# Kernel optimization log

Measured on AMD Instinct MI355X. Metric: run time of the kernel, lower is better.

Reference implementation:

```python
import jax, jax.numpy as jnp
import numpy as np

N = 200000
B = 2
BEV_SIZES = [(376, 376), (188, 188), (94, 94), (188, 188), (94, 94)]
VOXELS = [40000, 20000, 10000, 20000, 10000]
IN_SCALES = 3
D_PT = 9        # point_feature_dim
D_AVFE = 64
D_AVFEO = 128
FINFO_MIN = float(np.finfo(np.float32).min)  # torch fills scatter_max output with finfo.min


def _make_vfs(V, H, W):
    # unique (batch, y, x) voxel coordinates for the dense scatter_nd
    total = B * H * W
    flat = np.arange(V, dtype=np.int64) * (total // V)
    b = flat // (H * W)
    r = flat % (H * W)
    return jnp.asarray(np.stack([b, r // W, r % W], axis=1), dtype=jnp.int32)


def setup_inputs():
    key = jax.random.key(0)
    ks = jax.random.split(key, 16)
    inp = {"points": jax.random.normal(ks[0], (N, 4), jnp.float32)}
    for i in range(5):
        inp[f"vlc{i}"] = jax.random.uniform(ks[1 + i], (N, 3), jnp.float32)
        inp[f"pv{i}"] = jax.random.randint(ks[6 + i], (N,), 0, VOXELS[i], dtype=jnp.int32)
        inp[f"vfs{i}"] = _make_vfs(VOXELS[i], *BEV_SIZES[i])
    s = 0.05
    inp["W_avfe_point"] = jax.random.normal(ks[11], (D_PT, D_AVFE), jnp.float32) * s
    inp["W_avfe_att"] = jax.random.normal(ks[12], (2 * D_PT, D_AVFE), jnp.float32) * s
    inp["W_avfeo_point"] = jax.random.normal(ks[13], (IN_SCALES * 2 * D_AVFE, D_AVFEO), jnp.float32) * s
    inp["W_avfeo_att"] = jax.random.normal(ks[14], (2 * D_PT, D_AVFEO), jnp.float32) * s
    inp["batch_size"] = B
    return inp


def _seg_mean_gather(x, idx, V):
    # scatterMean: per-voxel mean gathered back to points -> [N, C]
    s = jax.ops.segment_sum(x, idx, num_segments=V)
    cnt = jax.ops.segment_sum(jnp.ones((x.shape[0], 1), x.dtype), idx, num_segments=V)
    return (s / jnp.maximum(cnt, 1.0))[idx]


def _seg_max(x, idx, V):
    # scatterMax with torch finfo.min init for empty voxels
    return jnp.maximum(jax.ops.segment_max(x, idx, num_segments=V), FINFO_MIN)


def _scale_inputs(points, vlc, pv, V):
    pm = _seg_mean_gather(points, pv, V)                      # [N,4]
    plc = points[:, :3] - pm[:, :3]                            # [N,3]
    pif = jnp.concatenate([points, plc, vlc[:, :2]], axis=1)   # [N,9]
    a2 = _seg_mean_gather(pif, pv, V)                          # [N,9]
    a1 = jnp.concatenate([plc, pif[:, 3:]], axis=1)            # [N,9]
    att = jnp.concatenate([a1, a2], axis=1)                    # [N,18]
    return pif, att


def _dense(vfs, feat, batch_size, H, W):
    # scatter_nd into [B,H,W,C] then channels-first
    out = jnp.zeros((batch_size, H, W, feat.shape[1]), feat.dtype)
    out = out.at[vfs[:, 0], vfs[:, 1], vfs[:, 2]].set(feat)
    return jnp.transpose(out, (0, 3, 1, 2))


def reference(points, vlc0, vlc1, vlc2, vlc3, vlc4,
              W_avfe_point, W_avfe_att, W_avfeo_point, W_avfeo_att,
              pv0, pv1, pv2, pv3, pv4,
              vfs0, vfs1, vfs2, vfs3, vfs4, batch_size):
    vlcs = [vlc0, vlc1, vlc2, vlc3, vlc4]
    pvs = [pv0, pv1, pv2, pv3, pv4]
    vfss = [vfs0, vfs1, vfs2, vfs3, vfs4]

    avfe = []
    for i in range(IN_SCALES):
        V = vfss[i].shape[0]
        pif, att = _scale_inputs(points, vlcs[i], pvs[i], V)
        pfc = pif @ W_avfe_point                 # [N,64]
        afc = att @ W_avfe_att                   # [N,64]
        final = afc * pfc
        vf = _seg_max(final, pvs[i], V)          # [V,64]
        avfe.append(jnp.concatenate([final, vf[pvs[i]]], axis=1))  # [N,128]

    feat = jnp.concatenate(avfe, axis=1)         # [N,384]
    pfc_o = feat @ W_avfeo_point                 # [N,128]

    outs = []
    for i in range(IN_SCALES, len(vfss)):
        V = vfss[i].shape[0]
        pif, att = _scale_inputs(points, vlcs[i], pvs[i], V)
        afc = att @ W_avfeo_att                  # [N,128]
        final = afc * pfc_o
        vf = _seg_max(final, pvs[i], V)          # [V,128]
        H, W = BEV_SIZES[i]
        outs.append(_dense(vfss[i], vf, batch_size, H, W))
    return tuple(outs)
```

## Files before the change

### kernel.cpp

```cpp
#include <hip/hip_runtime.h>
#include <stdint.h>

#define N_PTS 200000
#define HW3 35344
#define HW4 8836
#define OUT4_OFF 9048064
#define OUT_ELEMS 11310080
#define S_FLOATS 1000000
#define F_UINTS  2240000
#define G_USHORTS 3840000
#define G4_OFF 2560000
#define NB3 625
#define NB4 313
typedef unsigned short ushort_t;

__device__ __forceinline__ float bfbits2f(unsigned hbits16) {
  return __uint_as_float(hbits16 << 16);
}
__device__ __forceinline__ ushort_t f2bf(float f) {
  if (!(f == f)) return (ushort_t)0;
  unsigned u = __float_as_uint(f);
  if ((u & 0x7F800000u) == 0x7F800000u)
    return (ushort_t)(((u >> 16) & 0x8000u) | 0x7F7Fu);
  unsigned r = u + 0x7FFFu + ((u >> 16) & 1u);
  ushort_t h = (ushort_t)(r >> 16);
  if ((h & 0x7FFFu) == 0x7F80u) h = (ushort_t)((h & 0x8000u) | 0x7F7Fu);
  return h;
}
__device__ __forceinline__ unsigned enc16(unsigned h) {
  return (h & 0x8000u) ? (h ^ 0xFFFFu) : (h | 0x8000u);
}
__device__ __forceinline__ unsigned dec16(unsigned e) {
  return (e & 0x8000u) ? (e & 0x7FFFu) : (e ^ 0xFFFFu);
}

__device__ __forceinline__ void casMaxPair(unsigned* w, unsigned lo, unsigned hi) {
  unsigned old = *w;
  while (true) {
    unsigned clo = old & 0xFFFFu, chi = old >> 16;
    unsigned nlo = lo > clo ? lo : clo;
    unsigned nhi = hi > chi ? hi : chi;
    unsigned nw = nlo | (nhi << 16);
    if (nw == old) break;
    unsigned prev = atomicCAS(w, old, nw);
    if (prev == old) break;
    old = prev;
  }
}

struct ScaleArgs {
  const ushort_t* vlc[5];
  const int*      pv[5];
  float*          stats[5];
  unsigned*       vf16[3];
};

__global__ void k_init(unsigned* __restrict__ outw, unsigned* __restrict__ g) {
  int i = blockIdx.x * blockDim.x + threadIdx.x;
  if (i < S_FLOATS) { outw[i] = 0u; return; }
  if (i < S_FLOATS + F_UINTS) { outw[i] = 0x00800080u; return; }
  i -= S_FLOATS + F_UINTS;
  if (i < G_USHORTS / 2) g[i] = 0x00800080u;
}

__global__ void __launch_bounds__(256) k_segsum(const ushort4* __restrict__ points, ScaleArgs a) {
  int p = blockIdx.x * blockDim.x + threadIdx.x;
  if (p >= N_PTS) return;
  ushort4 pu = points[p];
  float px = bfbits2f(pu.x), py = bfbits2f(pu.y), pz = bfbits2f(pu.z), pw = bfbits2f(pu.w);
  #pragma unroll
  for (int s = 0; s < 5; s++) {
    int v = a.pv[s][p];
    float l0 = bfbits2f(a.vlc[s][3 * p + 0]);
    float l1 = bfbits2f(a.vlc[s][3 * p + 1]);
    float* st = a.stats[s] + (size_t)v * 10;
    atomicAdd(st + 0, px);
    atomicAdd(st + 1, py);
    atomicAdd(st + 2, pz);
    atomicAdd(st + 3, pw);
    atomicAdd(st + 4, l0);
    atomicAdd(st + 5, l1);
    atomicAdd(st + 9, 1.0f);
  }
}

__global__ void k_voxstats(ScaleArgs a) {
  int i = blockIdx.x * blockDim.x + threadIdx.x;
  int s, v;
  if      (i <  40000) { s = 0; v = i; }
  else if (i <  60000) { s = 1; v = i - 40000; }
  else if (i <  70000) { s = 2; v = i - 60000; }
  else if (i <  90000) { s = 3; v = i - 70000; }
  else if (i < 100000) { s = 4; v = i - 90000; }
  else return;
  float* st = a.stats[s] + (size_t)v * 10;
  float cnt = st[9];
  float c = fmaxf(cnt, 1.0f);
  float s0 = st[0], s1 = st[1], s2 = st[2], s3 = st[3], s4 = st[4], s5 = st[5];
  float pm0 = s0 / c, pm1 = s1 / c, pm2 = s2 / c, pm3 = s3 / c;
  float mp0 = (s0 - cnt * pm0) / c;
  float mp1 = (s1 - cnt * pm1) / c;
  float mp2 = (s2 - cnt * pm2) / c;
  float mv0 = s4 / c, mv1 = s5 / c;
  st[0] = pm0; st[1] = pm1; st[2] = pm2; st[3] = pm3;
  st[4] = mp0; st[5] = mp1; st[6] = mp2; st[7] = mv0; st[8] = mv1;
}

__global__ void __launch_bounds__(256) k_scale012(
    const ushort4* __restrict__ points, ScaleArgs a,
    const ushort_t* __restrict__ Wp,
    const ushort_t* __restrict__ Wa) {
  __shared__ float WpS[9 * 64];
  __shared__ float WaS[18 * 64];
  int tid = threadIdx.x;
  for (int i = tid; i < 9 * 64; i += 256)  WpS[i] = bfbits2f(Wp[i]);
  for (int i = tid; i < 18 * 64; i += 256) WaS[i] = bfbits2f(Wa[i]);
  __syncthreads();

  int p = blockIdx.x * blockDim.x + tid;
  if (p >= N_PTS) return;
  ushort4 pu = points[p];
  float px = bfbits2f(pu.x), py = bfbits2f(pu.y), pz = bfbits2f(pu.z), pw = bfbits2f(pu.w);
  #pragma unroll 1
  for (int s = 0; s < 3; s++) {
    int v = a.pv[s][p];
    const float* st = a.stats[s] + (size_t)v * 10;
    float a2[9];
    #pragma unroll
    for (int k = 0; k < 9; k++) a2[k] = st[k];
    float plc0 = px - a2[0], plc1 = py - a2[1], plc2 = pz - a2[2];
    float vl0 = bfbits2f(a.vlc[s][3 * p + 0]);
    float vl1 = bfbits2f(a.vlc[s][3 * p + 1]);
    float pif[9] = {px, py, pz, pw, plc0, plc1, plc2, vl0, vl1};
    float att[18] = {plc0, plc1, plc2, pw, plc0, plc1, plc2, vl0, vl1,
                     a2[0], a2[1], a2[2], a2[3], a2[4], a2[5], a2[6], a2[7], a2[8]};
    unsigned* vfw = a.vf16[s] + (size_t)v * 32;
    #pragma unroll 1
    for (int cb = 0; cb < 64; cb += 16) {
      float accp[16], acca[16];
      #pragma unroll
      for (int l = 0; l < 16; l++) { accp[l] = 0.0f; acca[l] = 0.0f; }
      #pragma unroll
      for (int k = 0; k < 9; k++) {
        float x = pif[k];
        #pragma unroll
        for (int l = 0; l < 16; l++) accp[l] = fmaf(x, WpS[k * 64 + cb + l], accp[l]);
      }
      #pragma unroll
      for (int k = 0; k < 18; k++) {
        float x = att[k];
        #pragma unroll
        for (int l = 0; l < 16; l++) acca[l] = fmaf(x, WaS[k * 64 + cb + l], acca[l]);
      }
      #pragma unroll
      for (int l = 0; l < 16; l += 2) {
        unsigned lo = enc16(f2bf(acca[l] * accp[l]));
        unsigned hi = enc16(f2bf(acca[l + 1] * accp[l + 1]));
        casMaxPair(vfw + ((cb + l) >> 1), lo, hi);
      }
    }
  }
}

struct K4Args {
  const ushort4* points;
  const ushort_t* vlc[5];
  const int* pv[5];
  const float* stats[5];
  const unsigned* vf16[3];
  ushort_t* G;
  const ushort_t* Wp;
  const ushort_t* Wa;
  const ushort_t* Wpo;
  const ushort_t* Wao;
};

__global__ void __launch_bounds__(256, 2) k_big(K4Args a) {
  __shared__ __align__(16) float A[64][68];
  __shared__ __align__(16) unsigned Bw16[64][64];
  __shared__ __align__(16) float WpS[9][64];
  __shared__ __align__(16) float WaS[18][64];
  __shared__ __align__(16) float attS[64][20];
  __shared__ int pvAll[5][64];

  int tid = threadIdx.x;
  int p0 = blockIdx.x * 64;

  for (int i = tid; i < 9 * 64; i += 256)   WpS[0][i]  = bfbits2f(a.Wp[i]);
  for (int i = tid; i < 18 * 64; i += 256)  WaS[0][i]  = bfbits2f(a.Wa[i]);
  if (tid < 64) {
    #pragma unroll
    for (int s = 0; s < 5; s++) pvAll[s][tid] = a.pv[s][p0 + tid];
  }
  float4 pt = make_float4(0.f, 0.f, 0.f, 0.f);
  if (tid < 64) {
    ushort4 pu = a.points[p0 + tid];
    pt = make_float4(bfbits2f(pu.x), bfbits2f(pu.y), bfbits2f(pu.z), bfbits2f(pu.w));
  }
  __syncthreads();

  int pr = tid & 7;
  int cg = tid >> 3;
  int cb4 = cg << 2;
  int cb2 = cg << 1;

  float acc[8][4];
  #pragma unroll
  for (int j = 0; j < 8; j++)
    #pragma unroll
    for (int l = 0; l < 4; l++) acc[j][l] = 0.0f;

  #pragma unroll 1
  for (int kc = 0; kc < 6; kc++) {
    {
      const uint4* src = (const uint4*)(a.Wpo + (size_t)kc * 64 * 128);
      uint4* dst = (uint4*)&Bw16[0][0];
      for (int i = tid; i < 1024; i += 256) dst[i] = src[i];
    }
    int s = kc >> 1;
    if ((kc & 1) == 0) {
      if (tid < 64) {
        int v = pvAll[s][tid];
        const float* st = a.stats[s] + (size_t)v * 10;
        float a2k[9];
        #pragma unroll
        for (int k = 0; k < 9; k++) a2k[k] = st[k];
        float vl0 = bfbits2f(a.vlc[s][3 * (p0 + tid) + 0]);
        float vl1 = bfbits2f(a.vlc[s][3 * (p0 + tid) + 1]);
        float* row = attS[tid];
        row[0] = pt.x; row[1] = pt.y; row[2] = pt.z; row[3] = pt.w;
        row[4] = pt.x - a2k[0]; row[5] = pt.y - a2k[1]; row[6] = pt.z - a2k[2];
        row[7] = vl0; row[8] = vl1;
        #pragma unroll
        for (int k = 0; k < 9; k++) row[9 + k] = a2k[k];
      }
      __syncthreads();
      int p = tid >> 2, ch0 = (tid & 3) << 4;
      float pv_[18];
      #pragma unroll
      for (int k = 0; k < 18; k++) pv_[k] = attS[p][k];
      float accp[16], acca[16];
      #pragma unroll
      for (int l = 0; l < 16; l++) { accp[l] = 0.0f; acca[l] = 0.0f; }
      #pragma unroll
      for (int k = 0; k < 9; k++) {
        float x = pv_[k];
        #pragma unroll
        for (int l = 0; l < 16; l++) accp[l] = fmaf(x, WpS[k][ch0 + l], accp[l]);
      }
      #pragma unroll
      for (int k = 0; k < 18; k++) {
        int src = (k < 3) ? (4 + k) : (k == 3) ? 3 : k;
        float x = pv_[src];
        #pragma unroll
        for (int l = 0; l < 16; l++) acca[l] = fmaf(x, WaS[k][ch0 + l], acca[l]);
      }
      #pragma unroll
      for (int l4 = 0; l4 < 16; l4 += 4) {
        float4 f;
        f.x = accp[l4 + 0] * acca[l4 + 0];
        f.y = accp[l4 + 1] * acca[l4 + 1];
        f.z = accp[l4 + 2] * acca[l4 + 2];
        f.w = accp[l4 + 3] * acca[l4 + 3];
        *(float4*)&A[p][ch0 + l4] = f;
      }
    } else {
      const unsigned* vfw = a.vf16[s];
      for (int i = tid; i < 2048; i += 256) {
        int p = i >> 5; int wd = i & 31;
        int v = pvAll[s][p];
        unsigned q = vfw[(size_t)v * 32 + wd];
        A[p][2 * wd]     = bfbits2f(dec16(q & 0xFFFFu));
        A[p][2 * wd + 1] = bfbits2f(dec16(q >> 16));
      }
    }
    __syncthreads();
    #pragma unroll 2
    for (int kk = 0; kk < 64; kk += 4) {
      float4 av[8];
      #pragma unroll
      for (int j = 0; j < 8; j++) av[j] = *(const float4*)&A[pr + (j << 3)][kk];
      #pragma unroll
      for (int t = 0; t < 4; t++) {
        unsigned w0 = Bw16[kk + t][cb2], w1 = Bw16[kk + t][cb2 + 1];
        float b0 = __uint_as_float(w0 << 16);
        float b1 = __uint_as_float(w0 & 0xFFFF0000u);
        float b2 = __uint_as_float(w1 << 16);
        float b3 = __uint_as_float(w1 & 0xFFFF0000u);
        #pragma unroll
        for (int j = 0; j < 8; j++) {
          float x = (t == 0) ? av[j].x : (t == 1) ? av[j].y : (t == 2) ? av[j].z : av[j].w;
          acc[j][0] = fmaf(x, b0, acc[j][0]);
          acc[j][1] = fmaf(x, b1, acc[j][1]);
          acc[j][2] = fmaf(x, b2, acc[j][2]);
          acc[j][3] = fmaf(x, b3, acc[j][3]);
        }
      }
    }
    __syncthreads();
  }

  float* WaoE = &A[0][0];
  for (int i = tid; i < 18 * 128; i += 256) WaoE[i] = bfbits2f(a.Wao[i]);

  #pragma unroll 1
  for (int si = 0; si < 2; si++) {
    if (tid < 64) {
      int v = pvAll[3 + si][tid];
      const float* st = a.stats[3 + si] + (size_t)v * 10;
      float a2k[9];
      #pragma unroll
      for (int k = 0; k < 9; k++) a2k[k] = st[k];
      float vl0 = bfbits2f(a.vlc[3 + si][3 * (p0 + tid) + 0]);
      float vl1 = bfbits2f(a.vlc[3 + si][3 * (p0 + tid) + 1]);
      float plc0 = pt.x - a2k[0], plc1 = pt.y - a2k[1], plc2 = pt.z - a2k[2];
      float* row = attS[tid];
      row[0] = plc0; row[1] = plc1; row[2] = plc2; row[3] = pt.w;
      row[4] = plc0; row[5] = plc1; row[6] = plc2; row[7] = vl0; row[8] = vl1;
      #pragma unroll
      for (int k = 0; k < 9; k++) row[9 + k] = a2k[k];
    }
    __syncthreads();
    size_t gbase = si ? (size_t)G4_OFF : 0;
    float afc[8][4];
    #pragma unroll
    for (int j = 0; j < 8; j++)
      #pragma unroll
      for (int l = 0; l < 4; l++) afc[j][l] = 0.0f;
    #pragma unroll
    for (int k = 0; k < 18; k++) {
      float4 w = *(const float4*)&WaoE[k * 128 + cb4];
      #pragma unroll
      for (int j = 0; j < 8; j++) {
        float x = attS[pr + (j << 3)][k];
        afc[j][0] = fmaf(x, w.x, afc[j][0]);
        afc[j][1] = fmaf(x, w.y, afc[j][1]);
        afc[j][2] = fmaf(x, w.z, afc[j][2]);
        afc[j][3] = fmaf(x, w.w, afc[j][3]);
      }
    }
    #pragma unroll
    for (int j = 0; j < 8; j++) {
      int p = pr + (j << 3);
      int v = pvAll[3 + si][p];
      unsigned* gw = (unsigned*)a.G + ((gbase + (size_t)v * 128 + cb4) >> 1);
      unsigned e0 = enc16(f2bf(afc[j][0] * acc[j][0]));
      unsigned e1 = enc16(f2bf(afc[j][1] * acc[j][1]));
      unsigned e2 = enc16(f2bf(afc[j][2] * acc[j][2]));
      unsigned e3 = enc16(f2bf(afc[j][3] * acc[j][3]));
      casMaxPair(gw, e0, e1);
      casMaxPair(gw + 1, e2, e3);
    }
    __syncthreads();
  }
}

__global__ void k_clear(unsigned* __restrict__ outw) {
  int i = blockIdx.x * blockDim.x + threadIdx.x;
  if (i < OUT_ELEMS / 2) outw[i] = 0u;
}

__global__ void __launch_bounds__(256) k_scatter_out(const ushort_t* __restrict__ G,
                                                     const int* __restrict__ vfs3,
                                                     const int* __restrict__ vfs4,
                                                     ushort_t* __restrict__ out16) {
  __shared__ ushort_t tile[32][130];
  __shared__ int vbase[32];
  int blk = blockIdx.x;
  int s = (blk >= NB3) ? 1 : 0;
  int v0 = (s ? (blk - NB3) : blk) * 32;
  int V = s ? 10000 : 20000;
  int HW = s ? HW4 : HW3;
  int W = s ? 94 : 188;
  const int* vfs = s ? vfs4 : vfs3;
  size_t goff = s ? (size_t)G4_OFF : 0;
  size_t ooff = s ? (size_t)OUT4_OFF : 0;
  int nv = min(32, V - v0);
  int tid = threadIdx.x;
  const unsigned* gw = (const unsigned*)(G + goff);
  for (int i = tid; i < nv * 64; i += 256) {
    int vi = i >> 6, cw = i & 63;
    unsigned q = gw[(size_t)(v0 + vi) * 64 + cw];
    tile[vi][2 * cw]     = (ushort_t)(q & 0xFFFFu);
    tile[vi][2 * cw + 1] = (ushort_t)(q >> 16);
  }
  if (tid < nv) {
    int v = v0 + tid;
    int b = vfs[3 * v], y = vfs[3 * v + 1], x = vfs[3 * v + 2];
    vbase[tid] = (b * 128) * HW + y * W + x;
  }
  __syncthreads();
  for (int i = tid; i < 128 * 32; i += 256) {
    int c = i >> 5, vi = i & 31;
    if (vi < nv) {
      unsigned d = dec16(tile[vi][c]);
      if ((d & 0x7F80u) == 0x7F80u) d = (d & 0x8000u) | 0x7F7Fu;
      out16[ooff + (size_t)vbase[vi] + (size_t)c * HW] = (ushort_t)d;
    }
  }
}

extern "C" void kernel_launch(void* const* d_in, const int* in_sizes, int n_in,
                              void* d_out, int out_size, void* d_ws, size_t ws_size,
                              hipStream_t stream) {
  static const int VOX[5] = {40000, 20000, 10000, 20000, 10000};

  const ushort_t* points = (const ushort_t*)d_in[0];
  const ushort_t* vlc[5]; const int* pv[5]; const int* vfs[5];
  const ushort_t *Wp, *Wa, *Wpo, *Wao;
  if (in_sizes[2] == N_PTS) {
    for (int s = 0; s < 5; s++) {
      vlc[s] = (const ushort_t*)d_in[1 + 3 * s];
      pv[s]  = (const int*)     d_in[2 + 3 * s];
      vfs[s] = (const int*)     d_in[3 + 3 * s];
    }
    Wp  = (const ushort_t*)d_in[16];
    Wa  = (const ushort_t*)d_in[17];
    Wpo = (const ushort_t*)d_in[18];
    Wao = (const ushort_t*)d_in[19];
  } else {
    for (int s = 0; s < 5; s++) vlc[s] = (const ushort_t*)d_in[1 + s];
    Wp  = (const ushort_t*)d_in[6];
    Wa  = (const ushort_t*)d_in[7];
    Wpo = (const ushort_t*)d_in[8];
    Wao = (const ushort_t*)d_in[9];
    for (int s = 0; s < 5; s++) pv[s]  = (const int*)d_in[10 + s];
    for (int s = 0; s < 5; s++) vfs[s] = (const int*)d_in[15 + s];
  }

  float* statsBase = (float*)d_out;
  unsigned* outw = (unsigned*)d_out;
  unsigned* fBase = outw + S_FLOATS;
  ushort_t* G = (ushort_t*)d_ws;
  ushort_t* out16 = (ushort_t*)d_out;

  float* stats[5];
  size_t offS = 0;
  for (int s = 0; s < 5; s++) { stats[s] = statsBase + offS; offS += (size_t)VOX[s] * 10; }
  unsigned* vf16[3];
  size_t offF = 0;
  for (int s = 0; s < 3; s++) { vf16[s] = fBase + offF; offF += (size_t)VOX[s] * 32; }

  ScaleArgs sa;
  for (int s = 0; s < 5; s++) { sa.vlc[s] = vlc[s]; sa.pv[s] = pv[s]; sa.stats[s] = stats[s]; }
  for (int s = 0; s < 3; s++) sa.vf16[s] = vf16[s];

  int totInit = S_FLOATS + F_UINTS + G_USHORTS / 2;
  k_init<<<(totInit + 255) / 256, 256, 0, stream>>>(outw, (unsigned*)d_ws);

  k_segsum<<<(N_PTS + 255) / 256, 256, 0, stream>>>((const ushort4*)points, sa);

  k_voxstats<<<(100000 + 255) / 256, 256, 0, stream>>>(sa);

  k_scale012<<<(N_PTS + 255) / 256, 256, 0, stream>>>((const ushort4*)points, sa, Wp, Wa);

  K4Args ka;
  ka.points = (const ushort4*)points;
  for (int s = 0; s < 5; s++) { ka.vlc[s] = vlc[s]; ka.pv[s] = pv[s]; ka.stats[s] = stats[s]; }
  for (int s = 0; s < 3; s++) ka.vf16[s] = vf16[s];
  ka.G = G;
  ka.Wp = Wp; ka.Wa = Wa; ka.Wpo = Wpo; ka.Wao = Wao;
  k_big<<<N_PTS / 64, 256, 0, stream>>>(ka);

  k_clear<<<(OUT_ELEMS / 2 + 255) / 256, 256, 0, stream>>>(outw);

  k_scatter_out<<<NB3 + NB4, 256, 0, stream>>>(G, vfs[3], vfs[4], out16);
}
```

Baseline: 1.567 ms.

## Double k_big point tile, read Wpo from global, use 64-bit CAS max

```diff
diff --git a/kernel.cpp b/kernel.cpp
--- a/kernel.cpp
+++ b/kernel.cpp
@@ -13,6 +13,7 @@
 #define NB3 625
 #define NB4 313
 typedef unsigned short ushort_t;
+typedef unsigned long long u64;
 
 __device__ __forceinline__ float bfbits2f(unsigned hbits16) {
   return __uint_as_float(hbits16 << 16);
@@ -34,15 +35,18 @@
   return (e & 0x8000u) ? (e & 0x7FFFu) : (e ^ 0xFFFFu);
 }
 
-__device__ __forceinline__ void casMaxPair(unsigned* w, unsigned lo, unsigned hi) {
-  unsigned old = *w;
+__device__ __forceinline__ void casMax64(u64* w, u64 enc) {
+  u64 old = *w;
   while (true) {
-    unsigned clo = old & 0xFFFFu, chi = old >> 16;
-    unsigned nlo = lo > clo ? lo : clo;
-    unsigned nhi = hi > chi ? hi : chi;
-    unsigned nw = nlo | (nhi << 16);
+    u64 nw = 0;
+    #pragma unroll
+    for (int i = 0; i < 4; i++) {
+      u64 m = 0xFFFFull << (i * 16);
+      u64 av = old & m, bv = enc & m;
+      nw |= (av > bv) ? av : bv;
+    }
     if (nw == old) break;
-    unsigned prev = atomicCAS(w, old, nw);
+    u64 prev = atomicCAS(w, old, nw);
     if (prev == old) break;
     old = prev;
   }
@@ -153,10 +157,12 @@
         for (int l = 0; l < 16; l++) acca[l] = fmaf(x, WaS[k * 64 + cb + l], acca[l]);
       }
       #pragma unroll
-      for (int l = 0; l < 16; l += 2) {
-        unsigned lo = enc16(f2bf(acca[l] * accp[l]));
-        unsigned hi = enc16(f2bf(acca[l + 1] * accp[l + 1]));
-        casMaxPair(vfw + ((cb + l) >> 1), lo, hi);
+      for (int l = 0; l < 16; l += 4) {
+        u64 e = (u64)enc16(f2bf(acca[l] * accp[l]))
+              | ((u64)enc16(f2bf(acca[l + 1] * accp[l + 1])) << 16)
+              | ((u64)enc16(f2bf(acca[l + 2] * accp[l + 2])) << 32)
+              | ((u64)enc16(f2bf(acca[l + 3] * accp[l + 3])) << 48);
+        casMax64((u64*)(vfw + ((cb + l) >> 1)), e);
       }
     }
   }
@@ -175,26 +181,24 @@
   const ushort_t* Wao;
 };
 
-__global__ void __launch_bounds__(256, 2) k_big(K4Args a) {
-  __shared__ __align__(16) float A[64][68];
-  __shared__ __align__(16) unsigned Bw16[64][64];
+__global__ void __launch_bounds__(256, 3) k_big(K4Args a) {
+  __shared__ __align__(16) float A[128][68];
   __shared__ __align__(16) float WpS[9][64];
   __shared__ __align__(16) float WaS[18][64];
-  __shared__ __align__(16) float attS[64][20];
-  __shared__ int pvAll[5][64];
+  __shared__ __align__(16) float attS[128][20];
+  __shared__ int pvAll[5][128];
 
   int tid = threadIdx.x;
-  int p0 = blockIdx.x * 64;
+  int p0 = blockIdx.x * 128;
+  int pIdx = min(p0 + tid, N_PTS - 1);
 
   for (int i = tid; i < 9 * 64; i += 256)   WpS[0][i]  = bfbits2f(a.Wp[i]);
   for (int i = tid; i < 18 * 64; i += 256)  WaS[0][i]  = bfbits2f(a.Wa[i]);
-  if (tid < 64) {
-    #pragma unroll
-    for (int s = 0; s < 5; s++) pvAll[s][tid] = a.pv[s][p0 + tid];
-  }
   float4 pt = make_float4(0.f, 0.f, 0.f, 0.f);
-  if (tid < 64) {
-    ushort4 pu = a.points[p0 + tid];
+  if (tid < 128) {
+    #pragma unroll
+    for (int s = 0; s < 5; s++) pvAll[s][tid] = a.pv[s][pIdx];
+    ushort4 pu = a.points[pIdx];
     pt = make_float4(bfbits2f(pu.x), bfbits2f(pu.y), bfbits2f(pu.z), bfbits2f(pu.w));
   }
   __syncthreads();
@@ -202,31 +206,27 @@
   int pr = tid & 7;
   int cg = tid >> 3;
   int cb4 = cg << 2;
-  int cb2 = cg << 1;
-
-  float acc[8][4];
+
+  float acc[16][4];
   #pragma unroll
-  for (int j = 0; j < 8; j++)
+  for (int j = 0; j < 16; j++)
     #pragma unroll
     for (int l = 0; l < 4; l++) acc[j][l] = 0.0f;
+
+  const uint2* Bg = (const uint2*)a.Wpo;
 
   #pragma unroll 1
   for (int kc = 0; kc < 6; kc++) {
-    {
-      const uint4* src = (const uint4*)(a.Wpo + (size_t)kc * 64 * 128);
-      uint4* dst = (uint4*)&Bw16[0][0];
-      for (int i = tid; i < 1024; i += 256) dst[i] = src[i];
-    }
     int s = kc >> 1;
     if ((kc & 1) == 0) {
-      if (tid < 64) {
+      if (tid < 128) {
         int v = pvAll[s][tid];
         const float* st = a.stats[s] + (size_t)v * 10;
         float a2k[9];
         #pragma unroll
         for (int k = 0; k < 9; k++) a2k[k] = st[k];
-        float vl0 = bfbits2f(a.vlc[s][3 * (p0 + tid) + 0]);
-        float vl1 = bfbits2f(a.vlc[s][3 * (p0 + tid) + 1]);
+        float vl0 = bfbits2f(a.vlc[s][3 * pIdx + 0]);
+        float vl1 = bfbits2f(a.vlc[s][3 * pIdx + 1]);
         float* row = attS[tid];
         row[0] = pt.x; row[1] = pt.y; row[2] = pt.z; row[3] = pt.w;
         row[4] = pt.x - a2k[0]; row[5] = pt.y - a2k[1]; row[6] = pt.z - a2k[2];
@@ -235,38 +235,41 @@
         for (int k = 0; k < 9; k++) row[9 + k] = a2k[k];
       }
       __syncthreads();
-      int p = tid >> 2, ch0 = (tid & 3) << 4;
-      float pv_[18];
-      #pragma unroll
-      for (int k = 0; k < 18; k++) pv_[k] = attS[p][k];
-      float accp[16], acca[16];
-      #pragma unroll
-      for (int l = 0; l < 16; l++) { accp[l] = 0.0f; acca[l] = 0.0f; }
-      #pragma unroll
-      for (int k = 0; k < 9; k++) {
-        float x = pv_[k];
-        #pragma unroll
-        for (int l = 0; l < 16; l++) accp[l] = fmaf(x, WpS[k][ch0 + l], accp[l]);
-      }
-      #pragma unroll
-      for (int k = 0; k < 18; k++) {
-        int src = (k < 3) ? (4 + k) : (k == 3) ? 3 : k;
-        float x = pv_[src];
-        #pragma unroll
-        for (int l = 0; l < 16; l++) acca[l] = fmaf(x, WaS[k][ch0 + l], acca[l]);
-      }
-      #pragma unroll
-      for (int l4 = 0; l4 < 16; l4 += 4) {
-        float4 f;
-        f.x = accp[l4 + 0] * acca[l4 + 0];
-        f.y = accp[l4 + 1] * acca[l4 + 1];
-        f.z = accp[l4 + 2] * acca[l4 + 2];
-        f.w = accp[l4 + 3] * acca[l4 + 3];
-        *(float4*)&A[p][ch0 + l4] = f;
+      #pragma unroll 1
+      for (int pp = 0; pp < 2; pp++) {
+        int p = pp * 64 + (tid >> 2), ch0 = (tid & 3) << 4;
+        float pv_[18];
+        #pragma unroll
+        for (int k = 0; k < 18; k++) pv_[k] = attS[p][k];
+        float accp[16], acca[16];
+        #pragma unroll
+        for (int l = 0; l < 16; l++) { accp[l] = 0.0f; acca[l] = 0.0f; }
+        #pragma unroll
+        for (int k = 0; k < 9; k++) {
+          float x = pv_[k];
+          #pragma unroll
+          for (int l = 0; l < 16; l++) accp[l] = fmaf(x, WpS[k][ch0 + l], accp[l]);
+        }
+        #pragma unroll
+        for (int k = 0; k < 18; k++) {
+          int src = (k < 3) ? (4 + k) : (k == 3) ? 3 : k;
+          float x = pv_[src];
+          #pragma unroll
+          for (int l = 0; l < 16; l++) acca[l] = fmaf(x, WaS[k][ch0 + l], acca[l]);
+        }
+        #pragma unroll
+        for (int l4 = 0; l4 < 16; l4 += 4) {
+          float4 f;
+          f.x = accp[l4 + 0] * acca[l4 + 0];
+          f.y = accp[l4 + 1] * acca[l4 + 1];
+          f.z = accp[l4 + 2] * acca[l4 + 2];
+          f.w = accp[l4 + 3] * acca[l4 + 3];
+          *(float4*)&A[p][ch0 + l4] = f;
+        }
       }
     } else {
       const unsigned* vfw = a.vf16[s];
-      for (int i = tid; i < 2048; i += 256) {
+      for (int i = tid; i < 4096; i += 256) {
         int p = i >> 5; int wd = i & 31;
         int v = pvAll[s][p];
         unsigned q = vfw[(size_t)v * 32 + wd];
@@ -275,25 +278,35 @@
       }
     }
     __syncthreads();
-    #pragma unroll 2
+    #pragma unroll 1
     for (int kk = 0; kk < 64; kk += 4) {
-      float4 av[8];
-      #pragma unroll
-      for (int j = 0; j < 8; j++) av[j] = *(const float4*)&A[pr + (j << 3)][kk];
+      uint2 bw[4];
+      #pragma unroll
+      for (int t = 0; t < 4; t++) bw[t] = Bg[(size_t)(kc * 64 + kk + t) * 32 + cg];
+      float bf[4][4];
       #pragma unroll
       for (int t = 0; t < 4; t++) {
-        unsigned w0 = Bw16[kk + t][cb2], w1 = Bw16[kk + t][cb2 + 1];
-        float b0 = __uint_as_float(w0 << 16);
-        float b1 = __uint_as_float(w0 & 0xFFFF0000u);
-        float b2 = __uint_as_float(w1 << 16);
-        float b3 = __uint_as_float(w1 & 0xFFFF0000u);
-        #pragma unroll
-        for (int j = 0; j < 8; j++) {
-          float x = (t == 0) ? av[j].x : (t == 1) ? av[j].y : (t == 2) ? av[j].z : av[j].w;
-          acc[j][0] = fmaf(x, b0, acc[j][0]);
-          acc[j][1] = fmaf(x, b1, acc[j][1]);
-          acc[j][2] = fmaf(x, b2, acc[j][2]);
-          acc[j][3] = fmaf(x, b3, acc[j][3]);
+        bf[t][0] = __uint_as_float(bw[t].x << 16);
+        bf[t][1] = __uint_as_float(bw[t].x & 0xFFFF0000u);
+        bf[t][2] = __uint_as_float(bw[t].y << 16);
+        bf[t][3] = __uint_as_float(bw[t].y & 0xFFFF0000u);
+      }
+      #pragma unroll
+      for (int jh = 0; jh < 2; jh++) {
+        float4 av[8];
+        #pragma unroll
+        for (int j8 = 0; j8 < 8; j8++) av[j8] = *(const float4*)&A[pr + ((jh * 8 + j8) << 3)][kk];
+        #pragma unroll
+        for (int t = 0; t < 4; t++) {
+          #pragma unroll
+          for (int j8 = 0; j8 < 8; j8++) {
+            float x = (t == 0) ? av[j8].x : (t == 1) ? av[j8].y : (t == 2) ? av[j8].z : av[j8].w;
+            int j = jh * 8 + j8;
+            acc[j][0] = fmaf(x, bf[t][0], acc[j][0]);
+            acc[j][1] = fmaf(x, bf[t][1], acc[j][1]);
+            acc[j][2] = fmaf(x, bf[t][2], acc[j][2]);
+            acc[j][3] = fmaf(x, bf[t][3], acc[j][3]);
+          }
         }
       }
     }
@@ -305,14 +318,14 @@
 
   #pragma unroll 1
   for (int si = 0; si < 2; si++) {
-    if (tid < 64) {
+    if (tid < 128) {
       int v = pvAll[3 + si][tid];
       const float* st = a.stats[3 + si] + (size_t)v * 10;
       float a2k[9];
       #pragma unroll
       for (int k = 0; k < 9; k++) a2k[k] = st[k];
-      float vl0 = bfbits2f(a.vlc[3 + si][3 * (p0 + tid) + 0]);
-      float vl1 = bfbits2f(a.vlc[3 + si][3 * (p0 + tid) + 1]);
+      float vl0 = bfbits2f(a.vlc[3 + si][3 * pIdx + 0]);
+      float vl1 = bfbits2f(a.vlc[3 + si][3 * pIdx + 1]);
       float plc0 = pt.x - a2k[0], plc1 = pt.y - a2k[1], plc2 = pt.z - a2k[2];
       float* row = attS[tid];
       row[0] = plc0; row[1] = plc1; row[2] = plc2; row[3] = pt.w;
@@ -322,16 +335,16 @@
     }
     __syncthreads();
     size_t gbase = si ? (size_t)G4_OFF : 0;
-    float afc[8][4];
-    #pragma unroll
-    for (int j = 0; j < 8; j++)
+    float afc[16][4];
+    #pragma unroll
+    for (int j = 0; j < 16; j++)
       #pragma unroll
       for (int l = 0; l < 4; l++) afc[j][l] = 0.0f;
-    #pragma unroll
+    #pragma unroll 1
     for (int k = 0; k < 18; k++) {
       float4 w = *(const float4*)&WaoE[k * 128 + cb4];
       #pragma unroll
-      for (int j = 0; j < 8; j++) {
+      for (int j = 0; j < 16; j++) {
         float x = attS[pr + (j << 3)][k];
         afc[j][0] = fmaf(x, w.x, afc[j][0]);
         afc[j][1] = fmaf(x, w.y, afc[j][1]);
@@ -340,16 +353,14 @@
       }
     }
     #pragma unroll
-    for (int j = 0; j < 8; j++) {
+    for (int j = 0; j < 16; j++) {
       int p = pr + (j << 3);
       int v = pvAll[3 + si][p];
-      unsigned* gw = (unsigned*)a.G + ((gbase + (size_t)v * 128 + cb4) >> 1);
-      unsigned e0 = enc16(f2bf(afc[j][0] * acc[j][0]));
-      unsigned e1 = enc16(f2bf(afc[j][1] * acc[j][1]));
-      unsigned e2 = enc16(f2bf(afc[j][2] * acc[j][2]));
-      unsigned e3 = enc16(f2bf(afc[j][3] * acc[j][3]));
-      casMaxPair(gw, e0, e1);
-      casMaxPair(gw + 1, e2, e3);
+      u64 e = (u64)enc16(f2bf(afc[j][0] * acc[j][0]))
+            | ((u64)enc16(f2bf(afc[j][1] * acc[j][1])) << 16)
+            | ((u64)enc16(f2bf(afc[j][2] * acc[j][2])) << 32)
+            | ((u64)enc16(f2bf(afc[j][3] * acc[j][3])) << 48);
+      casMax64((u64*)(a.G + gbase + (size_t)v * 128 + cb4), e);
     }
     __syncthreads();
   }
@@ -460,7 +471,7 @@
   for (int s = 0; s < 3; s++) ka.vf16[s] = vf16[s];
   ka.G = G;
   ka.Wp = Wp; ka.Wa = Wa; ka.Wpo = Wpo; ka.Wao = Wao;
-  k_big<<<N_PTS / 64, 256, 0, stream>>>(ka);
+  k_big<<<(N_PTS + 127) / 128, 256, 0, stream>>>(ka);
 
   k_clear<<<(OUT_ELEMS / 2 + 255) / 256, 256, 0, stream>>>(outw);
 
```

After: 2.386 ms. +52.2%, slower.

## Use 64-bit CAS max packing four bf16 and read Wpo from global

Applied to the files above, without the earlier changes.

```diff
diff --git a/kernel.cpp b/kernel.cpp
--- a/kernel.cpp
+++ b/kernel.cpp
@@ -13,6 +13,7 @@
 #define NB3 625
 #define NB4 313
 typedef unsigned short ushort_t;
+typedef unsigned long long u64;
 
 __device__ __forceinline__ float bfbits2f(unsigned hbits16) {
   return __uint_as_float(hbits16 << 16);
@@ -34,15 +35,18 @@
   return (e & 0x8000u) ? (e & 0x7FFFu) : (e ^ 0xFFFFu);
 }
 
-__device__ __forceinline__ void casMaxPair(unsigned* w, unsigned lo, unsigned hi) {
-  unsigned old = *w;
+__device__ __forceinline__ void casMax64(u64* w, u64 enc) {
+  u64 old = *w;
   while (true) {
-    unsigned clo = old & 0xFFFFu, chi = old >> 16;
-    unsigned nlo = lo > clo ? lo : clo;
-    unsigned nhi = hi > chi ? hi : chi;
-    unsigned nw = nlo | (nhi << 16);
+    u64 nw = 0;
+    #pragma unroll
+    for (int i = 0; i < 4; i++) {
+      u64 m = 0xFFFFull << (i * 16);
+      u64 av = old & m, bv = enc & m;
+      nw |= (av > bv) ? av : bv;
+    }
     if (nw == old) break;
-    unsigned prev = atomicCAS(w, old, nw);
+    u64 prev = atomicCAS(w, old, nw);
     if (prev == old) break;
     old = prev;
   }
@@ -153,10 +157,12 @@
         for (int l = 0; l < 16; l++) acca[l] = fmaf(x, WaS[k * 64 + cb + l], acca[l]);
       }
       #pragma unroll
-      for (int l = 0; l < 16; l += 2) {
-        unsigned lo = enc16(f2bf(acca[l] * accp[l]));
-        unsigned hi = enc16(f2bf(acca[l + 1] * accp[l + 1]));
-        casMaxPair(vfw + ((cb + l) >> 1), lo, hi);
+      for (int l = 0; l < 16; l += 4) {
+        u64 e = (u64)enc16(f2bf(acca[l] * accp[l]))
+              | ((u64)enc16(f2bf(acca[l + 1] * accp[l + 1])) << 16)
+              | ((u64)enc16(f2bf(acca[l + 2] * accp[l + 2])) << 32)
+              | ((u64)enc16(f2bf(acca[l + 3] * accp[l + 3])) << 48);
+        casMax64((u64*)(vfw + ((cb + l) >> 1)), e);
       }
     }
   }
@@ -175,9 +181,8 @@
   const ushort_t* Wao;
 };
 
-__global__ void __launch_bounds__(256, 2) k_big(K4Args a) {
+__global__ void __launch_bounds__(256, 3) k_big(K4Args a) {
   __shared__ __align__(16) float A[64][68];
-  __shared__ __align__(16) unsigned Bw16[64][64];
   __shared__ __align__(16) float WpS[9][64];
   __shared__ __align__(16) float WaS[18][64];
   __shared__ __align__(16) float attS[64][20];
@@ -202,7 +207,6 @@
   int pr = tid & 7;
   int cg = tid >> 3;
   int cb4 = cg << 2;
-  int cb2 = cg << 1;
 
   float acc[8][4];
   #pragma unroll
@@ -210,13 +214,10 @@
     #pragma unroll
     for (int l = 0; l < 4; l++) acc[j][l] = 0.0f;
 
+  const uint2* Bg = (const uint2*)a.Wpo;
+
   #pragma unroll 1
   for (int kc = 0; kc < 6; kc++) {
-    {
-      const uint4* src = (const uint4*)(a.Wpo + (size_t)kc * 64 * 128);
-      uint4* dst = (uint4*)&Bw16[0][0];
-      for (int i = tid; i < 1024; i += 256) dst[i] = src[i];
-    }
     int s = kc >> 1;
     if ((kc & 1) == 0) {
       if (tid < 64) {
@@ -277,16 +278,18 @@
     __syncthreads();
     #pragma unroll 2
     for (int kk = 0; kk < 64; kk += 4) {
+      uint2 bw[4];
+      #pragma unroll
+      for (int t = 0; t < 4; t++) bw[t] = Bg[(size_t)(kc * 64 + kk + t) * 32 + cg];
       float4 av[8];
       #pragma unroll
       for (int j = 0; j < 8; j++) av[j] = *(const float4*)&A[pr + (j << 3)][kk];
       #pragma unroll
       for (int t = 0; t < 4; t++) {
-        unsigned w0 = Bw16[kk + t][cb2], w1 = Bw16[kk + t][cb2 + 1];
-        float b0 = __uint_as_float(w0 << 16);
-        float b1 = __uint_as_float(w0 & 0xFFFF0000u);
-        float b2 = __uint_as_float(w1 << 16);
-        float b3 = __uint_as_float(w1 & 0xFFFF0000u);
+        float b0 = __uint_as_float(bw[t].x << 16);
+        float b1 = __uint_as_float(bw[t].x & 0xFFFF0000u);
+        float b2 = __uint_as_float(bw[t].y << 16);
+        float b3 = __uint_as_float(bw[t].y & 0xFFFF0000u);
         #pragma unroll
         for (int j = 0; j < 8; j++) {
           float x = (t == 0) ? av[j].x : (t == 1) ? av[j].y : (t == 2) ? av[j].z : av[j].w;
@@ -343,13 +346,11 @@
     for (int j = 0; j < 8; j++) {
       int p = pr + (j << 3);
       int v = pvAll[3 + si][p];
-      unsigned* gw = (unsigned*)a.G + ((gbase + (size_t)v * 128 + cb4) >> 1);
-      unsigned e0 = enc16(f2bf(afc[j][0] * acc[j][0]));
-      unsigned e1 = enc16(f2bf(afc[j][1] * acc[j][1]));
-      unsigned e2 = enc16(f2bf(afc[j][2] * acc[j][2]));
-      unsigned e3 = enc16(f2bf(afc[j][3] * acc[j][3]));
-      casMaxPair(gw, e0, e1);
-      casMaxPair(gw + 1, e2, e3);
+      u64 e = (u64)enc16(f2bf(afc[j][0] * acc[j][0]))
+            | ((u64)enc16(f2bf(afc[j][1] * acc[j][1])) << 16)
+            | ((u64)enc16(f2bf(afc[j][2] * acc[j][2])) << 32)
+            | ((u64)enc16(f2bf(afc[j][3] * acc[j][3])) << 48);
+      casMax64((u64*)(a.G + gbase + (size_t)v * 128 + cb4), e);
     }
     __syncthreads();
   }
```

After: 1.662 ms. +6.0%, slower.
